# Kernel optimization log

Hardware: AMD Instinct MI355X
Metric: run time of the kernel (lower is better)

The kernel has to match this reference:

```python
import jax, jax.numpy as jnp
import numpy as np
from jax.scipy.special import logsumexp

NUM_TAGS = 32
START_TAG = 30
STOP_TAG = 31
NEG_INF = -10000.0


def setup_inputs() -> dict:
    key = jax.random.key(0)
    k1, k2 = jax.random.split(key)
    B, S, T = 2048, 512, NUM_TAGS
    input_features = jax.random.normal(k1, (B, S, T), dtype=jnp.float32)
    transitions = jax.random.normal(k2, (T, T), dtype=jnp.float32)
    # transitions[to, from]; never transition INTO start, never FROM stop
    transitions = transitions.at[START_TAG, :].set(NEG_INF)
    transitions = transitions.at[:, STOP_TAG].set(NEG_INF)
    return {"input_features": input_features, "transitions": transitions}


def reference(input_features, transitions):
    """Linear-chain CRF forward algorithm: log partition function per batch.

    input_features: [B, S, T] emission scores
    transitions:    [T, T], transitions[i, j] = score of j -> i
    returns:        [B] log Z
    """
    B, S, T = input_features.shape
    alpha0 = jnp.full((B, T), NEG_INF, dtype=input_features.dtype)
    alpha0 = alpha0.at[:, START_TAG].set(0.0)

    emits = jnp.swapaxes(input_features, 0, 1)  # [S, B, T]

    def step(alpha, emit_t):
        # scores[b, i, j] = alpha[b, j] + transitions[i, j]
        next_alpha = logsumexp(alpha[:, None, :] + transitions[None, :, :], axis=2)
        return next_alpha + emit_t, None

    alpha, _ = jax.lax.scan(step, alpha0, emits)
    # terminate: transition to STOP_TAG
    log_z = logsumexp(alpha + transitions[STOP_TAG][None, :], axis=1)  # [B]
    return log_z
```

## Files before the change

kernel.cpp:

```cpp
#include <hip/hip_runtime.h>


constexpr int SEQ = 512;
constexpr int NTAGS = 32;
constexpr int START_TAG = 30;
constexpr int STOP_TAG = 31;
constexpr float LOG2E = 1.4426950408889634f;
constexpr float LN2 = 0.6931471805599453f;

#if __has_builtin(__builtin_amdgcn_exp2f)
#define EXP2(x) __builtin_amdgcn_exp2f(x)
#else
#define EXP2(x) exp2f(x)
#endif
#if __has_builtin(__builtin_amdgcn_logf)
#define LOG2(x) __builtin_amdgcn_logf(x)
#else
#define LOG2(x) log2f(x)
#endif

__global__ __launch_bounds__(64, 8) void crf_fwd_kernel(
    const float* __restrict__ feat, const float* __restrict__ trans,
    float* __restrict__ out) {
  const int tid = threadIdx.x;
  const int h = tid >> 5;
  const int i = tid & 31;
  const int b = blockIdx.x;

  __shared__ union {
    float f[NTAGS];
    float4 v[NTAGS / 4];
  } pb;

  float E[16];
#pragma unroll
  for (int k = 0; k < 16; ++k)
    E[k] = EXP2(trans[i * 32 + h * 16 + k] * LOG2E);
  const float tstop = trans[STOP_TAG * 32 + i] * LOG2E;

  float s = (i == START_TAG) ? 0.0f : -14427.0f;
  float zacc = 0.0f;
  float r = 0.0f;

  const float* Fp = feat + (size_t)b * (SEQ * NTAGS) + i;
  float em[16];
#pragma unroll
  for (int u = 0; u < 16; ++u) em[u] = Fp[u * 32];
  Fp += 16 * 32;

  auto step = [&](float emv) {
    float p = EXP2(s);
    pb.f[i] = p;
    float4 q0 = pb.v[h * 4 + 0];
    float4 q1 = pb.v[h * 4 + 1];
    float4 q2 = pb.v[h * 4 + 2];
    float4 q3 = pb.v[h * 4 + 3];
    float a0 = E[0] * q0.x;
    a0 = fmaf(E[1], q0.y, a0); a0 = fmaf(E[2], q0.z, a0); a0 = fmaf(E[3], q0.w, a0);
    float a1 = E[4] * q1.x;
    a1 = fmaf(E[5], q1.y, a1); a1 = fmaf(E[6], q1.z, a1); a1 = fmaf(E[7], q1.w, a1);
    float a2 = E[8] * q2.x;
    a2 = fmaf(E[9], q2.y, a2); a2 = fmaf(E[10], q2.z, a2); a2 = fmaf(E[11], q2.w, a2);
    float a3 = E[12] * q3.x;
    a3 = fmaf(E[13], q3.y, a3); a3 = fmaf(E[14], q3.z, a3); a3 = fmaf(E[15], q3.w, a3);
    float acc = (a0 + a1) + (a2 + a3);
    acc += __shfl_xor(acc, 32, 64);
    float anew = LOG2(acc);
    anew = fmaf(emv, LOG2E, anew);
    anew -= r;
    zacc += r;
    s = anew;
    r = __int_as_float(__builtin_amdgcn_readfirstlane(__float_as_int(anew)));
  };

  for (int blk = 0; blk < 31; ++blk) {
#pragma unroll
    for (int u = 0; u < 16; ++u) {
      step(em[u]);
      em[u] = Fp[u * 32];
    }
    Fp += 16 * 32;
  }
#pragma unroll
  for (int u = 0; u < 16; ++u) step(em[u]);

  float pe = EXP2(s + tstop);
#pragma unroll
  for (int m = 16; m >= 1; m >>= 1) pe += __shfl_xor(pe, m, 64);
  if (tid == 0) out[b] = (LOG2(pe) + zacc) * LN2;
}

extern "C" void kernel_launch(void* const* d_in, const int* in_sizes, int n_in,
                              void* d_out, int out_size, void* d_ws,
                              size_t ws_size, hipStream_t stream) {
  const float* feat = (const float*)d_in[0];
  const float* trans = (const float*)d_in[1];
  float* out = (float*)d_out;
  const int B = in_sizes[0] / (SEQ * NTAGS);
  crf_fwd_kernel<<<B, 64, 0, stream>>>(feat, trans, out);
}
```

Measured before the change: 217.4 us.

## Parallelize CRF scan over sequence chunks with bf16 MFMA transfer-matrix products

Rewrites the forward recursion as products of 32x32 transfer matrices in linear space. Each of 8 waves computes the product for a 64-step chunk with bf16 MFMA and periodic power-of-two renormalisation. Wave 0 then chains the chunk matrices to get log Z. This removes the strict 512-step serial dependency per batch row and turns per-step dot products into matrix-core work. The cost is bf16 precision loss in the accumulated products, plus the scaling bookkeeping and a final LDS combine.

```diff
diff --git a/kernel.cpp b/kernel.cpp
--- a/kernel.cpp
+++ b/kernel.cpp
@@ -1,4 +1,5 @@
 #include <hip/hip_runtime.h>
+#include <hip/hip_bf16.h>
 
 
 constexpr int SEQ = 512;
@@ -7,6 +8,12 @@
 constexpr int STOP_TAG = 31;
 constexpr float LOG2E = 1.4426950408889634f;
 constexpr float LN2 = 0.6931471805599453f;
+constexpr int CHUNK = 64;
+constexpr int NWAVE = 8;
+
+typedef float f32x16 __attribute__((ext_vector_type(16)));
+typedef short bf16x8 __attribute__((ext_vector_type(8)));
+typedef int i32x4 __attribute__((ext_vector_type(4)));
 
 #if __has_builtin(__builtin_amdgcn_exp2f)
 #define EXP2(x) __builtin_amdgcn_exp2f(x)
@@ -19,75 +26,142 @@
 #define LOG2(x) log2f(x)
 #endif
 
-__global__ __launch_bounds__(64, 8) void crf_fwd_kernel(
+static __device__ __forceinline__ int bf16pk(float lo, float hi) {
+  union { __hip_bfloat162 v; int i; } u;
+  u.v.x = __float2bfloat16(lo);
+  u.v.y = __float2bfloat16(hi);
+  return u.i;
+}
+
+__global__ __launch_bounds__(NWAVE * 64, 4) void crf_fwd_mfma(
     const float* __restrict__ feat, const float* __restrict__ trans,
     float* __restrict__ out) {
   const int tid = threadIdx.x;
-  const int h = tid >> 5;
-  const int i = tid & 31;
+  const int w = tid >> 6;
+  const int lane = tid & 63;
+  const int h = lane >> 5;
+  const int mi = lane & 31;
   const int b = blockIdx.x;
 
-  __shared__ union {
-    float f[NTAGS];
-    float4 v[NTAGS / 4];
-  } pb;
+  __shared__ float Tl[NWAVE][32 * 32];
+  __shared__ float sig[NWAVE];
+  __shared__ float pv[NTAGS];
 
-  float E[16];
+  int rowq[16];
 #pragma unroll
-  for (int k = 0; k < 16; ++k)
-    E[k] = EXP2(trans[i * 32 + h * 16 + k] * LOG2E);
-  const float tstop = trans[STOP_TAG * 32 + i] * LOG2E;
+  for (int q = 0; q < 16; ++q) rowq[q] = (q & 3) + 8 * (q >> 2) + 4 * h;
 
-  float s = (i == START_TAG) ? 0.0f : -14427.0f;
-  float zacc = 0.0f;
-  float r = 0.0f;
+  float ETp[16];
+#pragma unroll
+  for (int q = 0; q < 16; ++q)
+    ETp[q] = EXP2(LOG2E * trans[mi * 32 + rowq[q]]);
 
-  const float* Fp = feat + (size_t)b * (SEQ * NTAGS) + i;
-  float em[16];
+  int Bw[8];
 #pragma unroll
-  for (int u = 0; u < 16; ++u) em[u] = Fp[u * 32];
-  Fp += 16 * 32;
+  for (int r = 0; r < 8; ++r) {
+    int lo = (rowq[2 * r] == mi) ? 0x3F80 : 0;
+    int hi = (rowq[2 * r + 1] == mi) ? 0x3F80 : 0;
+    Bw[r] = lo | (hi << 16);
+  }
 
-  auto step = [&](float emv) {
-    float p = EXP2(s);
-    pb.f[i] = p;
-    float4 q0 = pb.v[h * 4 + 0];
-    float4 q1 = pb.v[h * 4 + 1];
-    float4 q2 = pb.v[h * 4 + 2];
-    float4 q3 = pb.v[h * 4 + 3];
-    float a0 = E[0] * q0.x;
-    a0 = fmaf(E[1], q0.y, a0); a0 = fmaf(E[2], q0.z, a0); a0 = fmaf(E[3], q0.w, a0);
-    float a1 = E[4] * q1.x;
-    a1 = fmaf(E[5], q1.y, a1); a1 = fmaf(E[6], q1.z, a1); a1 = fmaf(E[7], q1.w, a1);
-    float a2 = E[8] * q2.x;
-    a2 = fmaf(E[9], q2.y, a2); a2 = fmaf(E[10], q2.z, a2); a2 = fmaf(E[11], q2.w, a2);
-    float a3 = E[12] * q3.x;
-    a3 = fmaf(E[13], q3.y, a3); a3 = fmaf(E[14], q3.z, a3); a3 = fmaf(E[15], q3.w, a3);
-    float acc = (a0 + a1) + (a2 + a3);
-    acc += __shfl_xor(acc, 32, 64);
-    float anew = LOG2(acc);
-    anew = fmaf(emv, LOG2E, anew);
-    anew -= r;
-    zacc += r;
-    s = anew;
-    r = __int_as_float(__builtin_amdgcn_readfirstlane(__float_as_int(anew)));
+  const f32x16 zero = {};
+  f32x16 acc;
+  float sigma = 0.0f, nshift = 0.0f;
+
+  const float* Fp = feat + ((size_t)b * SEQ + (size_t)w * CHUNK) * NTAGS + mi;
+  float em[8];
+#pragma unroll
+  for (int u = 0; u < 8; ++u) em[u] = Fp[u * 32];
+  Fp += 8 * 32;
+
+  auto step = [&](float emv, float sh) {
+    float arg = fminf(fmaf(emv, LOG2E, sh), 120.0f);
+    float e2 = EXP2(arg);
+    int Aw[8];
+#pragma unroll
+    for (int r = 0; r < 8; ++r)
+      Aw[r] = bf16pk(e2 * ETp[2 * r], e2 * ETp[2 * r + 1]);
+    bf16x8 A0 = __builtin_bit_cast(bf16x8, (i32x4){Aw[0], Aw[1], Aw[2], Aw[3]});
+    bf16x8 A1 = __builtin_bit_cast(bf16x8, (i32x4){Aw[4], Aw[5], Aw[6], Aw[7]});
+    bf16x8 B0 = __builtin_bit_cast(bf16x8, (i32x4){Bw[0], Bw[1], Bw[2], Bw[3]});
+    bf16x8 B1 = __builtin_bit_cast(bf16x8, (i32x4){Bw[4], Bw[5], Bw[6], Bw[7]});
+    f32x16 c0 = __builtin_amdgcn_mfma_f32_32x32x16_bf16(A0, B0, zero, 0, 0, 0);
+    acc = __builtin_amdgcn_mfma_f32_32x32x16_bf16(A1, B1, c0, 0, 0, 0);
+#pragma unroll
+    for (int r = 0; r < 8; ++r) Bw[r] = bf16pk(acc[2 * r], acc[2 * r + 1]);
   };
 
-  for (int blk = 0; blk < 31; ++blk) {
+  auto renorm = [&]() {
+    float m = acc[0];
 #pragma unroll
-    for (int u = 0; u < 16; ++u) {
-      step(em[u]);
+    for (int q = 1; q < 16; ++q) m = fmaxf(m, acc[q]);
+#pragma unroll
+    for (int d = 1; d <= 32; d <<= 1) m = fmaxf(m, __shfl_xor(m, d, 64));
+    int eb = (__float_as_int(m) >> 23) & 0xFF;
+    sigma += (float)(eb - 127);
+    nshift = fminf(fmaxf((float)(127 - eb), -126.0f), 110.0f);
+  };
+
+  for (int blk = 0; blk < CHUNK / 8 - 1; ++blk) {
+#pragma unroll
+    for (int u = 0; u < 8; ++u) {
+      step(em[u], (u == 0 || u == 4) ? nshift : 0.0f);
+      if (u == 3) renorm();
       em[u] = Fp[u * 32];
     }
-    Fp += 16 * 32;
+    Fp += 8 * 32;
+    renorm();
   }
 #pragma unroll
-  for (int u = 0; u < 16; ++u) step(em[u]);
+  for (int u = 0; u < 8; ++u) {
+    step(em[u], (u == 0 || u == 4) ? nshift : 0.0f);
+    if (u == 3) renorm();
+  }
 
-  float pe = EXP2(s + tstop);
+  {
+    float m = acc[0];
 #pragma unroll
-  for (int m = 16; m >= 1; m >>= 1) pe += __shfl_xor(pe, m, 64);
-  if (tid == 0) out[b] = (LOG2(pe) + zacc) * LN2;
+    for (int q = 1; q < 16; ++q) m = fmaxf(m, acc[q]);
+#pragma unroll
+    for (int d = 1; d <= 32; d <<= 1) m = fmaxf(m, __shfl_xor(m, d, 64));
+    int eb = (__float_as_int(m) >> 23) & 0xFF;
+    if (eb < 1) eb = 1;
+    if (eb > 253) eb = 253;
+    sigma += (float)(eb - 127);
+    float g = __int_as_float((254 - eb) << 23);
+#pragma unroll
+    for (int q = 0; q < 16; ++q) acc[q] *= g;
+  }
+
+#pragma unroll
+  for (int q = 0; q < 16; ++q)
+    Tl[w][mi * 32 + (rowq[q] ^ mi)] = acc[q];
+  if (lane == 0) sig[w] = sigma;
+  __syncthreads();
+
+  if (w == 0) {
+    if (h == 0) pv[mi] = (mi == START_TAG) ? 1.0f : 0.0f;
+    float v = 0.0f;
+    for (int c = 0; c < NWAVE; ++c) {
+      v = 0.0f;
+#pragma unroll
+      for (int u = 0; u < 16; ++u) {
+        int j = 16 * h + u;
+        v = fmaf(Tl[c][j * 32 + (mi ^ j)], pv[j], v);
+      }
+      v += __shfl_xor(v, 32, 64);
+      if (h == 0) pv[mi] = v;
+    }
+    float stw = EXP2(LOG2E * trans[STOP_TAG * 32 + mi]);
+    float d = v * stw;
+#pragma unroll
+    for (int dd = 1; dd <= 16; dd <<= 1) d += __shfl_xor(d, dd, 64);
+    if (tid == 0) {
+      float sg = 0.0f;
+      for (int c2 = 0; c2 < NWAVE; ++c2) sg += sig[c2];
+      out[b] = LN2 * (LOG2(d) + sg);
+    }
+  }
 }
 
 extern "C" void kernel_launch(void* const* d_in, const int* in_sizes, int n_in,
@@ -97,5 +171,5 @@
   const float* trans = (const float*)d_in[1];
   float* out = (float*)d_out;
   const int B = in_sizes[0] / (SEQ * NTAGS);
-  crf_fwd_kernel<<<B, 64, 0, stream>>>(feat, trans, out);
+  crf_fwd_mfma<<<B, NWAVE * 64, 0, stream>>>(feat, trans, out);
 }
```

New measurement: 297.2 us. +36.7%, slower.
